# Kernel optimization log

Measured on AMD Instinct MI355X. Metric: run time of the kernel, lower is better.

Reference implementation:

```python
import jax, jax.numpy as jnp
import numpy as np

MARGIN = 5.0
VAR_FLOOR = 1e-4
BIG = 1e6


def setup_inputs() -> dict:
    key = jax.random.key(0)
    ks = jax.random.split(key, 8)
    B, D, R = 512, 768, 128
    C_new, C_old = 10, 100
    return {
        "features": jax.random.normal(ks[0], (B, D), jnp.float32),
        "labels": jax.random.randint(ks[1], (B,), 0, C_new),
        "new_class_ids": jnp.arange(C_new),
        "cur_means": jax.random.normal(ks[2], (C_new, D), jnp.float32),
        "cur_bases": jax.random.normal(ks[3], (C_new, D, R), jnp.float32),
        "cur_variances": jax.random.uniform(ks[4], (C_new, R + 1), jnp.float32),
        "calibrated_old_means": jax.random.normal(ks[5], (C_old, D), jnp.float32),
        "calibrated_old_bases": jax.random.normal(ks[6], (C_old, D, R), jnp.float32),
        "calibrated_old_variances": jax.random.uniform(ks[7], (C_old, R + 1), jnp.float32),
    }


def _geometry_distance_matrix(z, means, bases, variances):
    # z: [B,D], means: [C,D], bases: [C,D,R], variances: [C,R+1] -> [B,C]
    diff = z[:, None, :] - means[None, :, :]                    # [B,C,D]
    coeff = jnp.einsum('bcd,cdr->bcr', diff, bases)             # [B,C,R]
    eig = jnp.maximum(variances[:, :-1], VAR_FLOOR)             # [C,R]
    res = jnp.maximum(variances[:, -1], VAR_FLOOR)              # [C]
    parallel = jnp.sum(coeff * coeff / eig[None, :, :], axis=-1)  # [B,C]
    recon = jnp.einsum('bcr,cdr->bcd', coeff, bases)            # [B,C,D]
    residual_term = jnp.sum((diff - recon) ** 2, axis=-1) / res[None, :]
    dist = (parallel + residual_term) / z.shape[1]              # normalize_by_dim
    return jnp.nan_to_num(dist, nan=BIG, posinf=BIG, neginf=BIG)


def reference(features, labels, new_class_ids, cur_means, cur_bases, cur_variances,
              calibrated_old_means, calibrated_old_bases, calibrated_old_variances):
    z = jnp.nan_to_num(features, nan=0.0, posinf=0.0, neginf=0.0)  # [B,D]
    labels = labels.reshape(-1)

    own_all = _geometry_distance_matrix(z, cur_means, cur_bases, cur_variances)  # [B,C_new_total]
    old_all = _geometry_distance_matrix(z, calibrated_old_means, calibrated_old_bases,
                                        calibrated_old_variances)               # [B,C_old]
    old_min = jnp.min(old_all, axis=1)                                           # [B]

    # Per-new-class masks; union of class masks reproduces new_mask implicitly.
    masks = (labels[None, :] == new_class_ids[:, None]).astype(z.dtype)          # [K,B]
    counts = masks.sum(axis=1)                                                   # [K]
    denom = jnp.maximum(counts, 1.0)

    own_k = own_all[:, new_class_ids].T                                          # [K,B]
    hinge = jax.nn.relu(MARGIN + own_k - old_min[None, :])                       # [K,B]

    total_k = (hinge * masks).sum(axis=1) / denom
    own_k_mean = (own_k * masks).sum(axis=1) / denom
    old_k_mean = (old_min[None, :] * masks).sum(axis=1) / denom

    valid = (counts > 0).astype(z.dtype)
    n_valid = jnp.maximum(valid.sum(), 1.0)
    total = (total_k * valid).sum() / n_valid
    own = (own_k_mean * valid).sum() / n_valid
    old = (old_k_mean * valid).sum() / n_valid
    return jnp.stack([total, own, old])  # [total, own, old]
```

## Files before the change

kernel.cpp:

```cpp
#include <hip/hip_runtime.h>
#include <hip/hip_bf16.h>
#include <math.h>
#include <stdint.h>

#define B_N   512
#define D_N   768
#define R_N   128
#define C_NEW 10
#define C_OLD 100
#define C_TOT 110
#define MARGIN_F    5.0f
#define VAR_FLOOR_F 1e-4f
#define BIG_F       1e6f

typedef __bf16 bf16;
typedef __bf16 bf16x4 __attribute__((ext_vector_type(4)));
typedef __bf16 bf16x8 __attribute__((ext_vector_type(8)));
typedef float  f32x4  __attribute__((ext_vector_type(4)));

__device__ __forceinline__ float cleanf(float v) { return isfinite(v) ? v : 0.0f; }

__global__ __launch_bounds__(256)
void prep_zmu(const float* __restrict__ z,
              const float* __restrict__ cur_means, const float* __restrict__ old_means,
              bf16* __restrict__ zbf, float* __restrict__ znorm, float* __restrict__ munorm)
{
    const int tid = threadIdx.x, wave = tid >> 6, lane = tid & 63;
    __shared__ float s[4];

    if (blockIdx.x < 128) {
        const int b = blockIdx.x * 4 + wave;
        const float4* src = (const float4*)(z + (size_t)b * D_N);
        bf16x4* dst = (bf16x4*)(zbf + (size_t)b * D_N);
        float nrm = 0.f;
        #pragma unroll
        for (int i = 0; i < 3; ++i) {
            float4 v = src[lane + i * 64];
            v.x = cleanf(v.x); v.y = cleanf(v.y); v.z = cleanf(v.z); v.w = cleanf(v.w);
            nrm += v.x * v.x + v.y * v.y + v.z * v.z + v.w * v.w;
            bf16x4 w;
            w[0] = (bf16)v.x; w[1] = (bf16)v.y; w[2] = (bf16)v.z; w[3] = (bf16)v.w;
            dst[lane + i * 64] = w;
        }
        #pragma unroll
        for (int off = 32; off >= 1; off >>= 1) nrm += __shfl_xor(nrm, off, 64);
        if (lane == 0) znorm[b] = nrm;
        return;
    }

    const int c = blockIdx.x - 128;
    const float* mu = (c < C_NEW) ? cur_means + (size_t)c * D_N
                                  : old_means + (size_t)(c - C_NEW) * D_N;
    float p = 0.f;
    for (int d = tid; d < D_N; d += 256) p += mu[d] * mu[d];
    #pragma unroll
    for (int off = 32; off >= 1; off >>= 1) p += __shfl_xor(p, off, 64);
    if (lane == 0) s[wave] = p;
    __syncthreads();
    if (tid == 0) munorm[c] = s[0] + s[1] + s[2] + s[3];
}

__global__ __launch_bounds__(256)
void transpose_mc(const float* __restrict__ cur_bases, const float* __restrict__ old_bases,
                  const float* __restrict__ cur_means, const float* __restrict__ old_means,
                  bf16* __restrict__ basesT, float* __restrict__ m_c)
{
    const int dt = blockIdx.x, c = blockIdx.y;
    const float* Bc = (c < C_NEW) ? cur_bases + (size_t)c * D_N * R_N
                                  : old_bases + (size_t)(c - C_NEW) * D_N * R_N;
    const float* mu = (c < C_NEW) ? cur_means + (size_t)c * D_N
                                  : old_means + (size_t)(c - C_NEW) * D_N;
    __shared__ bf16 T[128][132];
    __shared__ float sMu[128];
    const int t = threadIdx.x;
    const int d0 = dt * 128;
    if (t < 128) sMu[t] = mu[d0 + t];

    #pragma unroll 4
    for (int it = 0; it < 16; ++it) {
        int q = it * 256 + t;
        int d = q >> 5, rr = (q & 31) * 4;
        float4 v = *(const float4*)(Bc + (size_t)(d0 + d) * R_N + rr);
        T[rr + 0][d] = (bf16)v.x;
        T[rr + 1][d] = (bf16)v.y;
        T[rr + 2][d] = (bf16)v.z;
        T[rr + 3][d] = (bf16)v.w;
    }
    __syncthreads();

    #pragma unroll 4
    for (int it = 0; it < 16; ++it) {
        int q = it * 256 + t;
        int r = q >> 5, dd = (q & 31) * 4;
        ushort4 w = *(const ushort4*)&T[r][dd];
        *(ushort4*)(basesT + (size_t)c * R_N * D_N + (size_t)r * D_N + d0 + dd) = w;
    }

    {
        int r = t & 127, dh = t >> 7;
        float p = 0.f;
        #pragma unroll 8
        for (int k = 0; k < 64; ++k) {
            int d = dh * 64 + k;
            p += sMu[d] * (float)T[r][d];
        }
        atomicAdd(&m_c[c * R_N + r], p);
    }
}

__global__ __launch_bounds__(256)
void gram(const bf16* __restrict__ basesT, bf16* __restrict__ G)
{
    const int hc = blockIdx.x, c = blockIdx.y;
    const bf16* Tc = basesT + (size_t)c * R_N * D_N;
    __shared__ bf16 sT[128][72];
    const int tid = threadIdx.x, wave = tid >> 6, lane = tid & 63;
    const int quad = lane >> 4, l15 = lane & 15;
    const int wr = (wave >> 1) * 64;
    const int wc = hc * 64 + (wave & 1) * 32;

    f32x4 acc[4][2];
    #pragma unroll
    for (int i = 0; i < 4; ++i)
        #pragma unroll
        for (int j = 0; j < 2; ++j) acc[i][j] = (f32x4)0.0f;

    for (int k0 = 0; k0 < D_N; k0 += 64) {
        __syncthreads();
        #pragma unroll
        for (int p = 0; p < 4; ++p) {
            int q = p * 256 + tid, row = q >> 3, u = q & 7;
            *(uint4*)(&sT[row][u * 8]) = *(const uint4*)(Tc + (size_t)row * D_N + k0 + u * 8);
        }
        __syncthreads();
        #pragma unroll
        for (int kk = 0; kk < 64; kk += 32) {
            bf16x8 af[4], bg[2];
            #pragma unroll
            for (int i = 0; i < 4; ++i) af[i] = *(const bf16x8*)(&sT[wr + 16 * i + l15][kk + quad * 8]);
            #pragma unroll
            for (int j = 0; j < 2; ++j) bg[j] = *(const bf16x8*)(&sT[wc + 16 * j + l15][kk + quad * 8]);
            #pragma unroll
            for (int i = 0; i < 4; ++i)
                #pragma unroll
                for (int j = 0; j < 2; ++j)
                    acc[i][j] = __builtin_amdgcn_mfma_f32_16x16x32_bf16(af[i], bg[j], acc[i][j], 0, 0, 0);
        }
    }
    #pragma unroll
    for (int i = 0; i < 4; ++i)
        #pragma unroll
        for (int j = 0; j < 2; ++j)
            #pragma unroll
            for (int reg = 0; reg < 4; ++reg) {
                int r = wr + 16 * i + quad * 4 + reg;
                int s = wc + 16 * j + l15;
                G[(size_t)c * 16384 + (size_t)r * 128 + s] = (bf16)acc[i][j][reg];
            }
}

#define PADC 136
#define SM_A   0
#define SM_B   18432
#define SM_G   0
#define SM_C   36864
#define SM_M   (36864 + 34816)
#define SM_INV (SM_M + 512)
#define SM_PAR (SM_INV + 512)
#define SM_CN  (SM_PAR + 512)
#define SM_Q   (SM_CN + 512)
#define SM_T2  (SM_Q + 512)
#define SM_MU  (SM_T2 + 3072)
#define SM_SZ  (SM_MU + 1536)

__global__ __launch_bounds__(256, 2)
void main_dist(const bf16* __restrict__ zbf, const bf16* __restrict__ basesT,
               const bf16* __restrict__ G, const float* __restrict__ m_c,
               const float* __restrict__ cur_vars, const float* __restrict__ old_vars,
               const float* __restrict__ cur_means, const float* __restrict__ old_means,
               const float* __restrict__ znorm, const float* __restrict__ munorm,
               float* __restrict__ gdist)
{
    const int mt = blockIdx.x, c = blockIdx.y;
    const int b0 = mt * 128;
    const float* vars = (c < C_NEW) ? cur_vars + (size_t)c * (R_N + 1)
                                    : old_vars + (size_t)(c - C_NEW) * (R_N + 1);
    const float* mu = (c < C_NEW) ? cur_means + (size_t)c * D_N
                                  : old_means + (size_t)(c - C_NEW) * D_N;
    __shared__ __align__(16) unsigned char smem[SM_SZ];
    bf16*  sA   = (bf16*)(smem + SM_A);
    bf16*  sB   = (bf16*)(smem + SM_B);
    bf16*  sG   = (bf16*)(smem + SM_G);
    bf16*  sC   = (bf16*)(smem + SM_C);
    float* sM   = (float*)(smem + SM_M);
    float* sInv = (float*)(smem + SM_INV);
    float* sPar = (float*)(smem + SM_PAR);
    float* sCn  = (float*)(smem + SM_CN);
    float* sQ   = (float*)(smem + SM_Q);
    float* sT2  = (float*)(smem + SM_T2);
    bf16*  sMuB = (bf16*)(smem + SM_MU);

    const int tid = threadIdx.x, wave = tid >> 6, lane = tid & 63;
    const int quad = lane >> 4, l15 = lane & 15;
    const int wr = (wave >> 1) * 64, wc = (wave & 1) * 64;

    if (tid < 128) {
        sM[tid]   = m_c[c * R_N + tid];
        sInv[tid] = 1.0f / fmaxf(vars[tid], VAR_FLOOR_F);
        sQ[tid]   = 0.0f;
    }
    for (int i = tid; i < D_N; i += 256) sMuB[i] = (bf16)mu[i];

    f32x4 acc1[4][4];
    #pragma unroll
    for (int i = 0; i < 4; ++i)
        #pragma unroll
        for (int j = 0; j < 4; ++j) acc1[i][j] = (f32x4)0.0f;
    float zd = 0.f;
    const int zrow = tid >> 1, zhalf = tid & 1;

    const bf16* Az = zbf + (size_t)b0 * D_N;
    const bf16* Bb = basesT + (size_t)c * R_N * D_N;
    for (int k0 = 0; k0 < D_N; k0 += 64) {
        __syncthreads();
        #pragma unroll
        for (int p = 0; p < 4; ++p) {
            int q = p * 256 + tid, row = q >> 3, u = q & 7;
            *(uint4*)(sA + row * 72 + u * 8) = *(const uint4*)(Az + (size_t)row * D_N + k0 + u * 8);
            *(uint4*)(sB + row * 72 + u * 8) = *(const uint4*)(Bb + (size_t)row * D_N + k0 + u * 8);
        }
        __syncthreads();
        #pragma unroll
        for (int kk = 0; kk < 64; kk += 32) {
            bf16x8 af[4], bg[4];
            #pragma unroll
            for (int i = 0; i < 4; ++i) af[i] = *(const bf16x8*)(sA + (wr + 16 * i + l15) * 72 + kk + quad * 8);
            #pragma unroll
            for (int j = 0; j < 4; ++j) bg[j] = *(const bf16x8*)(sB + (wc + 16 * j + l15) * 72 + kk + quad * 8);
            #pragma unroll
            for (int i = 0; i < 4; ++i)
                #pragma unroll
                for (int j = 0; j < 4; ++j)
                    acc1[i][j] = __builtin_amdgcn_mfma_f32_16x16x32_bf16(af[i], bg[j], acc1[i][j], 0, 0, 0);
        }
        {
            const bf16* zr = sA + zrow * 72 + zhalf * 32;
            const bf16* mr = sMuB + k0 + zhalf * 32;
            #pragma unroll
            for (int m = 0; m < 4; ++m) {
                bf16x8 a = *(const bf16x8*)(zr + m * 8);
                bf16x8 b = *(const bf16x8*)(mr + m * 8);
                #pragma unroll
                for (int e = 0; e < 8; ++e) zd += (float)a[e] * (float)b[e];
            }
        }
    }
    sT2[512 + tid] = zd;

    #pragma unroll
    for (int j = 0; j < 4; ++j) {
        float mcv = sM[wc + 16 * j + l15];
        #pragma unroll
        for (int i = 0; i < 4; ++i)
            #pragma unroll
            for (int reg = 0; reg < 4; ++reg) {
                float cv = acc1[i][j][reg] - mcv;
                acc1[i][j][reg] = cv;
                int row = wr + 16 * i + quad * 4 + reg;
                int col = wc + 16 * j + l15;
                sC[row * PADC + col] = (bf16)cv;
            }
    }
    __syncthreads();

    {
        int row = tid >> 1, half = tid & 1;
        float par = 0.f, cn = 0.f;
        #pragma unroll
        for (int m = 0; m < 8; ++m) {
            bf16x8 v = *(const bf16x8*)(sC + row * PADC + half * 64 + m * 8);
            #pragma unroll
            for (int e = 0; e < 8; ++e) {
                float f = (float)v[e];
                int col = half * 64 + m * 8 + e;
                cn  += f * f;
                par += f * f * sInv[col];
            }
        }
        sT2[tid] = par;
        sT2[256 + tid] = cn;
    }
    #pragma unroll
    for (int p = 0; p < 8; ++p) {
        int q = p * 256 + tid, s = q >> 4, u = q & 15;
        *(uint4*)(sG + s * PADC + u * 8) = *(const uint4*)(G + (size_t)c * 16384 + (size_t)s * 128 + u * 8);
    }
    __syncthreads();
    if (tid < 128) {
        sPar[tid] = sT2[tid * 2] + sT2[tid * 2 + 1];
        sCn[tid]  = sT2[256 + tid * 2] + sT2[256 + tid * 2 + 1];
    }

    f32x4 acc2[4][4];
    #pragma unroll
    for (int i = 0; i < 4; ++i)
        #pragma unroll
        for (int j = 0; j < 4; ++j) acc2[i][j] = (f32x4)0.0f;
    #pragma unroll
    for (int kc = 0; kc < 128; kc += 32) {
        bf16x8 af[4], bg[4];
        #pragma unroll
        for (int i = 0; i < 4; ++i) af[i] = *(const bf16x8*)(sC + (wr + 16 * i + l15) * PADC + kc + quad * 8);
        #pragma unroll
        for (int j = 0; j < 4; ++j) bg[j] = *(const bf16x8*)(sG + (wc + 16 * j + l15) * PADC + kc + quad * 8);
        #pragma unroll
        for (int i = 0; i < 4; ++i)
            #pragma unroll
            for (int j = 0; j < 4; ++j)
                acc2[i][j] = __builtin_amdgcn_mfma_f32_16x16x32_bf16(af[i], bg[j], acc2[i][j], 0, 0, 0);
    }

    #pragma unroll
    for (int i = 0; i < 4; ++i)
        #pragma unroll
        for (int reg = 0; reg < 4; ++reg) {
            float qp = 0.f;
            #pragma unroll
            for (int j = 0; j < 4; ++j) qp += acc2[i][j][reg] * acc1[i][j][reg];
            qp += __shfl_xor(qp, 1, 64);
            qp += __shfl_xor(qp, 2, 64);
            qp += __shfl_xor(qp, 4, 64);
            qp += __shfl_xor(qp, 8, 64);
            if (l15 == 0) atomicAdd(&sQ[wr + 16 * i + quad * 4 + reg], qp);
        }
    __syncthreads();

    if (tid < 128) {
        int b = b0 + tid;
        float zdot = sT2[512 + tid * 2] + sT2[512 + tid * 2 + 1];
        float nd2 = znorm[b] - 2.0f * zdot + munorm[c];
        float res = fmaxf(vars[R_N], VAR_FLOOR_F);
        float dist = (sPar[tid] + (nd2 - 2.0f * sCn[tid] + sQ[tid]) / res) / (float)D_N;
        if (!isfinite(dist)) dist = BIG_F;
        gdist[(size_t)b * C_TOT + c] = dist;
    }
}

__global__ __launch_bounds__(64)
void finalize_stage1(const float* __restrict__ gdist,
                     const int* __restrict__ labels,
                     const int* __restrict__ ncid,
                     float* __restrict__ acc)
{
    const int b = blockIdx.x * 64 + threadIdx.x;
    const float* row = gdist + (size_t)b * C_TOT;
    float mn = 3.4e38f;
    #pragma unroll
    for (int cc = C_NEW; cc < C_TOT; ++cc) mn = fminf(mn, row[cc]);
    const int lab = labels[b];
    #pragma unroll
    for (int k = 0; k < C_NEW; ++k) {
        if (lab == ncid[k]) {
            int col = min(max(ncid[k], 0), C_TOT - 1);
            float ow = row[col];
            atomicAdd(&acc[k * 4 + 0], 1.0f);
            atomicAdd(&acc[k * 4 + 1], fmaxf(0.0f, MARGIN_F + ow - mn));
            atomicAdd(&acc[k * 4 + 2], ow);
            atomicAdd(&acc[k * 4 + 3], mn);
        }
    }
}

__global__ __launch_bounds__(64)
void finalize_stage2(const float* __restrict__ acc, float* __restrict__ out)
{
    if (threadIdx.x == 0) {
        float total = 0.f, own = 0.f, old = 0.f, nv = 0.f;
        #pragma unroll
        for (int k = 0; k < C_NEW; ++k) {
            float cnt = acc[k * 4 + 0];
            float den = fmaxf(cnt, 1.0f);
            if (cnt > 0.f) {
                nv += 1.f;
                total += acc[k * 4 + 1] / den;
                own   += acc[k * 4 + 2] / den;
                old   += acc[k * 4 + 3] / den;
            }
        }
        float nvd = fmaxf(nv, 1.0f);
        out[0] = total / nvd;
        out[1] = own / nvd;
        out[2] = old / nvd;
    }
}

extern "C" void kernel_launch(void* const* d_in, const int* in_sizes, int n_in,
                              void* d_out, int out_size, void* d_ws, size_t ws_size,
                              hipStream_t stream)
{
    const float* features  = (const float*)d_in[0];
    const int*   labels    = (const int*)d_in[1];
    const int*   ncid      = (const int*)d_in[2];
    const float* cur_means = (const float*)d_in[3];
    const float* cur_bases = (const float*)d_in[4];
    const float* cur_vars  = (const float*)d_in[5];
    const float* old_means = (const float*)d_in[6];
    const float* old_bases = (const float*)d_in[7];
    const float* old_vars  = (const float*)d_in[8];

    unsigned char* ws = (unsigned char*)d_ws;
    float* gdist  = (float*)(ws + 0);
    bf16*  zbf    = (bf16*) (ws + 225280);
    float* znorm  = (float*)(ws + 1011712);
    float* munorm = (float*)(ws + 1013760);
    float* m_c    = (float*)(ws + 1014272);
    float* acc    = (float*)(ws + 1070592);
    bf16*  basesT = (bf16*) (ws + 1070848);
    bf16*  G      = (bf16*) (ws + 22697728);

    hipMemsetAsync(m_c, 0, 56320 + 256, stream);

    prep_zmu<<<dim3(128 + C_TOT), dim3(256), 0, stream>>>(features, cur_means, old_means,
                                                          zbf, znorm, munorm);
    transpose_mc<<<dim3(6, C_TOT), dim3(256), 0, stream>>>(cur_bases, old_bases,
                                                           cur_means, old_means,
                                                           basesT, m_c);
    gram<<<dim3(2, C_TOT), dim3(256), 0, stream>>>(basesT, G);
    main_dist<<<dim3(4, C_TOT), dim3(256), 0, stream>>>(zbf, basesT, G, m_c,
                                                        cur_vars, old_vars,
                                                        cur_means, old_means,
                                                        znorm, munorm, gdist);
    finalize_stage1<<<dim3(8), dim3(64), 0, stream>>>(gdist, labels, ncid, acc);
    finalize_stage2<<<dim3(1), dim3(64), 0, stream>>>(acc, (float*)d_out);
}
```

Baseline: 162.1 us.

## Fuse prep kernels, move mean projections into gram, merge finalize stages

Merges the z/mean prep and basis transpose into one kernel, moves the mean-norm and mean-projection (m_c) computation into the gram kernel's K loop, and folds the two finalize kernels into a single 512-thread block using shared-memory atomics. This removes the memset and two kernel launches, along with the global atomics on m_c and acc. In exchange, the gram hc==0 blocks do extra scalar work inside the MFMA loop and carry an extra 3 KB of shared memory. That creates imbalance between the two column-half blocks. A __syncthreads sits inside a branch on blockIdx, which is uniform per block, so it is safe.

```diff
diff --git a/kernel.cpp b/kernel.cpp
--- a/kernel.cpp
+++ b/kernel.cpp
@@ -21,12 +21,13 @@
 __device__ __forceinline__ float cleanf(float v) { return isfinite(v) ? v : 0.0f; }
 
 __global__ __launch_bounds__(256)
-void prep_zmu(const float* __restrict__ z,
-              const float* __restrict__ cur_means, const float* __restrict__ old_means,
-              bf16* __restrict__ zbf, float* __restrict__ znorm, float* __restrict__ munorm)
+void prep(const float* __restrict__ z,
+          const float* __restrict__ cur_bases, const float* __restrict__ old_bases,
+          bf16* __restrict__ zbf, float* __restrict__ znorm,
+          bf16* __restrict__ basesT)
 {
     const int tid = threadIdx.x, wave = tid >> 6, lane = tid & 63;
-    __shared__ float s[4];
+    __shared__ bf16 T[128][132];
 
     if (blockIdx.x < 128) {
         const int b = blockIdx.x * 4 + wave;
@@ -48,37 +49,15 @@
         return;
     }
 
-    const int c = blockIdx.x - 128;
-    const float* mu = (c < C_NEW) ? cur_means + (size_t)c * D_N
-                                  : old_means + (size_t)(c - C_NEW) * D_N;
-    float p = 0.f;
-    for (int d = tid; d < D_N; d += 256) p += mu[d] * mu[d];
-    #pragma unroll
-    for (int off = 32; off >= 1; off >>= 1) p += __shfl_xor(p, off, 64);
-    if (lane == 0) s[wave] = p;
-    __syncthreads();
-    if (tid == 0) munorm[c] = s[0] + s[1] + s[2] + s[3];
-}
-
-__global__ __launch_bounds__(256)
-void transpose_mc(const float* __restrict__ cur_bases, const float* __restrict__ old_bases,
-                  const float* __restrict__ cur_means, const float* __restrict__ old_means,
-                  bf16* __restrict__ basesT, float* __restrict__ m_c)
-{
-    const int dt = blockIdx.x, c = blockIdx.y;
+    const int pb = blockIdx.x - 128;
+    const int c = pb / 6, dt = pb % 6;
     const float* Bc = (c < C_NEW) ? cur_bases + (size_t)c * D_N * R_N
                                   : old_bases + (size_t)(c - C_NEW) * D_N * R_N;
-    const float* mu = (c < C_NEW) ? cur_means + (size_t)c * D_N
-                                  : old_means + (size_t)(c - C_NEW) * D_N;
-    __shared__ bf16 T[128][132];
-    __shared__ float sMu[128];
-    const int t = threadIdx.x;
     const int d0 = dt * 128;
-    if (t < 128) sMu[t] = mu[d0 + t];
 
     #pragma unroll 4
     for (int it = 0; it < 16; ++it) {
-        int q = it * 256 + t;
+        int q = it * 256 + tid;
         int d = q >> 5, rr = (q & 31) * 4;
         float4 v = *(const float4*)(Bc + (size_t)(d0 + d) * R_N + rr);
         T[rr + 0][d] = (bf16)v.x;
@@ -90,35 +69,37 @@
 
     #pragma unroll 4
     for (int it = 0; it < 16; ++it) {
-        int q = it * 256 + t;
+        int q = it * 256 + tid;
         int r = q >> 5, dd = (q & 31) * 4;
         ushort4 w = *(const ushort4*)&T[r][dd];
         *(ushort4*)(basesT + (size_t)c * R_N * D_N + (size_t)r * D_N + d0 + dd) = w;
     }
-
-    {
-        int r = t & 127, dh = t >> 7;
-        float p = 0.f;
-        #pragma unroll 8
-        for (int k = 0; k < 64; ++k) {
-            int d = dh * 64 + k;
-            p += sMu[d] * (float)T[r][d];
-        }
-        atomicAdd(&m_c[c * R_N + r], p);
-    }
 }
 
 __global__ __launch_bounds__(256)
-void gram(const bf16* __restrict__ basesT, bf16* __restrict__ G)
+void gram(const bf16* __restrict__ basesT,
+          const float* __restrict__ cur_means, const float* __restrict__ old_means,
+          bf16* __restrict__ G, float* __restrict__ m_c, float* __restrict__ munorm)
 {
     const int hc = blockIdx.x, c = blockIdx.y;
     const bf16* Tc = basesT + (size_t)c * R_N * D_N;
     __shared__ bf16 sT[128][72];
+    __shared__ float sMuF[D_N];
+    __shared__ float sRedW[4];
     const int tid = threadIdx.x, wave = tid >> 6, lane = tid & 63;
     const int quad = lane >> 4, l15 = lane & 15;
     const int wr = (wave >> 1) * 64;
     const int wc = hc * 64 + (wave & 1) * 32;
 
+    float muP = 0.f;
+    if (hc == 0) {
+        const float* mu = (c < C_NEW) ? cur_means + (size_t)c * D_N
+                                      : old_means + (size_t)(c - C_NEW) * D_N;
+        for (int d = tid; d < D_N; d += 256) { float v = mu[d]; sMuF[d] = v; muP += v * v; }
+    }
+    float mcAcc = 0.f;
+    const int mrow = tid >> 1, mhalf = tid & 1;
+
     f32x4 acc[4][2];
     #pragma unroll
     for (int i = 0; i < 4; ++i)
@@ -146,7 +127,23 @@
                 for (int j = 0; j < 2; ++j)
                     acc[i][j] = __builtin_amdgcn_mfma_f32_16x16x32_bf16(af[i], bg[j], acc[i][j], 0, 0, 0);
         }
-    }
+        if (hc == 0) {
+            #pragma unroll 8
+            for (int k = 0; k < 32; ++k)
+                mcAcc += sMuF[k0 + mhalf * 32 + k] * (float)sT[mrow][mhalf * 32 + k];
+        }
+    }
+
+    if (hc == 0) {
+        #pragma unroll
+        for (int off = 32; off >= 1; off >>= 1) muP += __shfl_xor(muP, off, 64);
+        if (lane == 0) sRedW[wave] = muP;
+        __syncthreads();
+        if (tid == 0) munorm[c] = sRedW[0] + sRedW[1] + sRedW[2] + sRedW[3];
+        mcAcc += __shfl_xor(mcAcc, 1, 64);
+        if (mhalf == 0) m_c[c * R_N + mrow] = mcAcc;
+    }
+
     #pragma unroll
     for (int i = 0; i < 4; ++i)
         #pragma unroll
@@ -346,45 +343,45 @@
     }
 }
 
-__global__ __launch_bounds__(64)
-void finalize_stage1(const float* __restrict__ gdist,
-                     const int* __restrict__ labels,
-                     const int* __restrict__ ncid,
-                     float* __restrict__ acc)
+__global__ __launch_bounds__(512)
+void finalize(const float* __restrict__ gdist,
+              const int* __restrict__ labels,
+              const int* __restrict__ ncid,
+              float* __restrict__ out)
 {
-    const int b = blockIdx.x * 64 + threadIdx.x;
-    const float* row = gdist + (size_t)b * C_TOT;
+    __shared__ float sAcc[C_NEW * 4];
+    const int tid = threadIdx.x;
+    if (tid < C_NEW * 4) sAcc[tid] = 0.f;
+    __syncthreads();
+
+    const float* row = gdist + (size_t)tid * C_TOT;
     float mn = 3.4e38f;
     #pragma unroll
     for (int cc = C_NEW; cc < C_TOT; ++cc) mn = fminf(mn, row[cc]);
-    const int lab = labels[b];
+    const int lab = labels[tid];
     #pragma unroll
     for (int k = 0; k < C_NEW; ++k) {
         if (lab == ncid[k]) {
             int col = min(max(ncid[k], 0), C_TOT - 1);
             float ow = row[col];
-            atomicAdd(&acc[k * 4 + 0], 1.0f);
-            atomicAdd(&acc[k * 4 + 1], fmaxf(0.0f, MARGIN_F + ow - mn));
-            atomicAdd(&acc[k * 4 + 2], ow);
-            atomicAdd(&acc[k * 4 + 3], mn);
-        }
-    }
-}
-
-__global__ __launch_bounds__(64)
-void finalize_stage2(const float* __restrict__ acc, float* __restrict__ out)
-{
-    if (threadIdx.x == 0) {
+            atomicAdd(&sAcc[k * 4 + 0], 1.0f);
+            atomicAdd(&sAcc[k * 4 + 1], fmaxf(0.0f, MARGIN_F + ow - mn));
+            atomicAdd(&sAcc[k * 4 + 2], ow);
+            atomicAdd(&sAcc[k * 4 + 3], mn);
+        }
+    }
+    __syncthreads();
+    if (tid == 0) {
         float total = 0.f, own = 0.f, old = 0.f, nv = 0.f;
         #pragma unroll
         for (int k = 0; k < C_NEW; ++k) {
-            float cnt = acc[k * 4 + 0];
+            float cnt = sAcc[k * 4 + 0];
             float den = fmaxf(cnt, 1.0f);
             if (cnt > 0.f) {
                 nv += 1.f;
-                total += acc[k * 4 + 1] / den;
-                own   += acc[k * 4 + 2] / den;
-                old   += acc[k * 4 + 3] / den;
+                total += sAcc[k * 4 + 1] / den;
+                own   += sAcc[k * 4 + 2] / den;
+                old   += sAcc[k * 4 + 3] / den;
             }
         }
         float nvd = fmaxf(nv, 1.0f);
@@ -414,22 +411,16 @@
     float* znorm  = (float*)(ws + 1011712);
     float* munorm = (float*)(ws + 1013760);
     float* m_c    = (float*)(ws + 1014272);
-    float* acc    = (float*)(ws + 1070592);
     bf16*  basesT = (bf16*) (ws + 1070848);
     bf16*  G      = (bf16*) (ws + 22697728);
 
-    hipMemsetAsync(m_c, 0, 56320 + 256, stream);
-
-    prep_zmu<<<dim3(128 + C_TOT), dim3(256), 0, stream>>>(features, cur_means, old_means,
-                                                          zbf, znorm, munorm);
-    transpose_mc<<<dim3(6, C_TOT), dim3(256), 0, stream>>>(cur_bases, old_bases,
-                                                           cur_means, old_means,
-                                                           basesT, m_c);
-    gram<<<dim3(2, C_TOT), dim3(256), 0, stream>>>(basesT, G);
+    prep<<<dim3(128 + 6 * C_TOT), dim3(256), 0, stream>>>(features, cur_bases, old_bases,
+                                                          zbf, znorm, basesT);
+    gram<<<dim3(2, C_TOT), dim3(256), 0, stream>>>(basesT, cur_means, old_means,
+                                                   G, m_c, munorm);
     main_dist<<<dim3(4, C_TOT), dim3(256), 0, stream>>>(zbf, basesT, G, m_c,
                                                         cur_vars, old_vars,
                                                         cur_means, old_means,
                                                         znorm, munorm, gdist);
-    finalize_stage1<<<dim3(8), dim3(64), 0, stream>>>(gdist, labels, ncid, acc);
-    finalize_stage2<<<dim3(1), dim3(64), 0, stream>>>(acc, (float*)d_out);
+    finalize<<<dim3(1), dim3(512), 0, stream>>>(gdist, labels, ncid, (float*)d_out);
 }
```

Measured after the change: 163.6 us. About the same (+0.9%).
